# Kernel tuning notes

Measured on AMD Instinct MI355X. Metric: run time of the kernel, lower is better.

The kernel has to match this reference:

```python
import jax, jax.numpy as jnp
import numpy as np

N, E = 10000, 30000
D_IN, E_DIM, H1, H2, C = 64, 16, 128, 64, 10


def setup_inputs() -> dict:
    key = jax.random.key(0)
    ks = jax.random.split(key, 12)
    x = jax.random.normal(ks[0], (N, D_IN), dtype=jnp.float32)
    edge_attr = jax.random.normal(ks[1], (E, E_DIM), dtype=jnp.float32)
    edge_index = jax.random.randint(ks[2], (2, E), 0, N, dtype=jnp.int64)
    # linear1: D_IN -> H1
    W1 = jax.random.normal(ks[3], (D_IN, H1), dtype=jnp.float32) / np.sqrt(D_IN)
    b1 = jnp.zeros((H1,), dtype=jnp.float32)
    # edge MLP 1: E_DIM -> H1*H2
    We1 = jax.random.normal(ks[4], (E_DIM, H1 * H2), dtype=jnp.float32) / np.sqrt(E_DIM)
    be1 = jnp.zeros((H1 * H2,), dtype=jnp.float32)
    root1 = jax.random.uniform(ks[5], (H1, H2), dtype=jnp.float32,
                               minval=-1.0 / np.sqrt(H1), maxval=1.0 / np.sqrt(H1))
    bias1 = jnp.zeros((H2,), dtype=jnp.float32)
    # edge MLP 2: E_DIM -> H2*C
    We2 = jax.random.normal(ks[6], (E_DIM, H2 * C), dtype=jnp.float32) / np.sqrt(E_DIM)
    be2 = jnp.zeros((H2 * C,), dtype=jnp.float32)
    root2 = jax.random.uniform(ks[7], (H2, C), dtype=jnp.float32,
                               minval=-1.0 / np.sqrt(H2), maxval=1.0 / np.sqrt(H2))
    bias2 = jnp.zeros((C,), dtype=jnp.float32)
    return {"x": x, "edge_attr": edge_attr, "edge_index": edge_index,
            "W1": W1, "b1": b1, "We1": We1, "be1": be1, "root1": root1, "bias1": bias1,
            "We2": We2, "be2": be2, "root2": root2, "bias2": bias2}


def _nnconv(h, src, dst, edge_attr, We, be, root, bias, c_in, c_out):
    # per-edge weight matrix from edge MLP: [E, c_in, c_out]
    W_e = (edge_attr @ We + be).reshape(-1, c_in, c_out)
    msg = jnp.einsum('ei,eio->eo', h[src], W_e)          # gather + batched matmul
    agg = jax.ops.segment_sum(msg, dst, num_segments=N)   # scatter-add to target nodes
    return agg + h @ root + bias


def reference(x, edge_attr, edge_index, W1, b1, We1, be1, root1, bias1,
              We2, be2, root2, bias2):
    src, dst = edge_index[0], edge_index[1]  # PyG: x_j = x[src], aggregate at dst
    h = jax.nn.relu(x @ W1 + b1)                               # [N, H1]
    h = jax.nn.relu(_nnconv(h, src, dst, edge_attr, We1, be1, root1, bias1, H1, H2))
    z = _nnconv(h, src, dst, edge_attr, We2, be2, root2, bias2, H2, C)
    return jax.nn.log_softmax(z, axis=1)
```

## Files before the change

### kernel.cpp

```cpp
#include <hip/hip_runtime.h>

#define N_NODES 10000
#define N_EDGES 30000
#define DIN     64
#define EDIM    16
#define H1      128
#define H2      64
#define C_OUT   10

typedef __bf16 bfrag __attribute__((ext_vector_type(8)));
typedef float  f32x4 __attribute__((ext_vector_type(4)));
typedef ushort ushort8 __attribute__((ext_vector_type(8)));

__device__ __forceinline__ ushort f2bf(float f) {
    union { float f; unsigned u; } x; x.f = f;
    unsigned r = x.u + 0x7fffu + ((x.u >> 16) & 1u);
    return (ushort)(r >> 16);
}
__device__ __forceinline__ float bf2f(ushort s) {
    union { unsigned u; float f; } x; x.u = ((unsigned)s) << 16;
    return x.f;
}

#define KA_B1   1250
#define KA_B2   (KA_B1 + 576)
#define KA_B3   (KA_B2 + 48)
__global__ __launch_bounds__(256) void kA_prep(
        const float* __restrict__ x, const float* __restrict__ W1,
        const float* __restrict__ b1,
        const float* __restrict__ We1, const float* __restrict__ root1,
        const float* __restrict__ be1,
        const float* __restrict__ We2, const float* __restrict__ be2,
        const float* __restrict__ root2,
        ushort* __restrict__ h_bf, ushort* __restrict__ B1t,
        ushort* __restrict__ B2t) {
    int t = threadIdx.x;
    int bx = blockIdx.x;
    if (bx < KA_B1) {
        __shared__ float w_lds[DIN * H1];
        __shared__ float b_lds[H1];
        __shared__ float x_lds[8][DIN];
        for (int idx = t; idx < DIN * H1 / 4; idx += 256)
            ((float4*)w_lds)[idx] = ((const float4*)W1)[idx];
        if (t < H1) b_lds[t] = b1[t];
        int n0 = bx * 8;
        if (t < 128) {
            int row = t >> 4, c4 = t & 15;
            int n = n0 + row;
            float4 v = make_float4(0.f, 0.f, 0.f, 0.f);
            if (n < N_NODES) v = ((const float4*)(x + (size_t)n * DIN))[c4];
            ((float4*)(x_lds[row]))[c4] = v;
        }
        __syncthreads();
        int nl = t >> 5;
        int o  = (t & 31) * 4;
        int n  = n0 + nl;
        float4 acc = *(const float4*)&b_lds[o];
        #pragma unroll 8
        for (int i = 0; i < DIN; ++i) {
            float xv = x_lds[nl][i];
            float4 w = *(const float4*)&w_lds[i * H1 + o];
            acc.x = fmaf(xv, w.x, acc.x);
            acc.y = fmaf(xv, w.y, acc.y);
            acc.z = fmaf(xv, w.z, acc.z);
            acc.w = fmaf(xv, w.w, acc.w);
        }
        if (n < N_NODES) {
            ushort4 s;
            s.x = f2bf(fmaxf(acc.x, 0.f));
            s.y = f2bf(fmaxf(acc.y, 0.f));
            s.z = f2bf(fmaxf(acc.z, 0.f));
            s.w = f2bf(fmaxf(acc.w, 0.f));
            *(ushort4*)&h_bf[(size_t)n * H1 + o] = s;
        }
    } else if (bx < KA_B2) {
        int idx = (bx - KA_B1) * 256 + t;
        int c = idx >> 7, i = idx & 127;
        float v;
        if (c < 1024) {
            int o = c >> 4, k = c & 15;
            v = We1[(size_t)k * (H1 * H2) + i * 64 + o];
        } else if (c < 1088) v = root1[i * 64 + (c - 1024)];
        else                 v = be1[i * 64 + (c - 1088)];
        B1t[idx] = f2bf(v);
    } else {
        int idx = (bx - KA_B2) * 256 + t;
        int c = idx >> 6, j = idx & 63;
        float v = 0.f;
        if (c < 160) {
            int cc = c >> 4, k = c & 15;
            v = We2[(size_t)k * 640 + j * 10 + cc];
        }
        else if (c < 170) v = be2[j * 10 + (c - 160)];
        else if (c < 180) v = root2[j * 10 + (c - 170)];
        B2t[idx] = f2bf(v);
    }
}

__global__ __launch_bounds__(256) void k3_mfma(
        const ushort* __restrict__ h_bf, const ushort* __restrict__ Bt,
        const float* __restrict__ bias1,
        ushort* __restrict__ G1t, float* __restrict__ hrb1, float* __restrict__ hb1,
        float* __restrict__ agg1, float* __restrict__ agg2) {
    int t = threadIdx.x;
    int wave = t >> 6, lane = t & 63;
    int quad = lane >> 4, lrow = lane & 15;
    int yy = blockIdx.y;
    int mx = blockIdx.x;
    if (yy == 5) {
        for (int i = mx * 256 + t; i < 160000; i += 79 * 256)
            ((float4*)agg1)[i] = make_float4(0.f, 0.f, 0.f, 0.f);
        for (int i = mx * 256 + t; i < 25000; i += 79 * 256)
            ((float4*)agg2)[i] = make_float4(0.f, 0.f, 0.f, 0.f);
    }
    int nbase = mx * 128 + wave * 32;
    int ar0 = nbase + lrow;       if (ar0 > N_NODES - 1) ar0 = N_NODES - 1;
    int ar1 = nbase + 16 + lrow;  if (ar1 > N_NODES - 1) ar1 = N_NODES - 1;
    bfrag A0[4], A1[4];
    #pragma unroll
    for (int kc4 = 0; kc4 < 4; ++kc4) {
        A0[kc4] = *reinterpret_cast<const bfrag*>(
            h_bf + (size_t)ar0 * 128 + kc4 * 32 + quad * 8);
        A1[kc4] = *reinterpret_cast<const bfrag*>(
            h_bf + (size_t)ar1 * 128 + kc4 * 32 + quad * 8);
    }
    #pragma unroll
    for (int hy = 0; hy < 3; ++hy) {
        int y = yy * 3 + hy;
        const ushort* bbase = Bt + (size_t)y * 64 * 128;
        f32x4 acc0[4] = {}, acc1[4] = {};
        #pragma unroll
        for (int kc4 = 0; kc4 < 4; ++kc4) {
            #pragma unroll
            for (int ct = 0; ct < 4; ++ct) {
                bfrag b = *reinterpret_cast<const bfrag*>(
                    bbase + (size_t)(ct * 16 + lrow) * 128 + kc4 * 32 + quad * 8);
                acc0[ct] = __builtin_amdgcn_mfma_f32_16x16x32_bf16(A0[kc4], b, acc0[ct], 0, 0, 0);
                acc1[ct] = __builtin_amdgcn_mfma_f32_16x16x32_bf16(A1[kc4], b, acc1[ct], 0, 0, 0);
            }
        }
        #pragma unroll
        for (int half = 0; half < 2; ++half) {
            int rbase = nbase + half * 16 + quad * 4;
            #pragma unroll
            for (int ct = 0; ct < 4; ++ct) {
                int col = ct * 16 + lrow;
                f32x4 a = half ? acc1[ct] : acc0[ct];
                #pragma unroll
                for (int r = 0; r < 4; ++r) {
                    int n = rbase + r;
                    if (n >= N_NODES) continue;
                    float v = a[r];
                    if (y < 16) {
                        G1t[(size_t)n * 1024 + y * 64 + col] = f2bf(v);
                    } else if (y == 16) {
                        hrb1[(size_t)n * 64 + col] = v + bias1[col];
                    } else {
                        hb1[(size_t)n * 64 + col] = v;
                    }
                }
            }
        }
    }
}

__global__ __launch_bounds__(256) void k4_edge1(
        const float* __restrict__ ea, const int* __restrict__ src_idx,
        const int* __restrict__ dst_idx, const ushort* __restrict__ G1t,
        const float* __restrict__ hb1, float* __restrict__ agg1) {
    int t = threadIdx.x;
    int e0 = blockIdx.x * 8 + (t >> 6) * 2;
    int o = t & 63;
    int s0 = src_idx[e0],     d0 = dst_idx[e0];
    int s1 = src_idx[e0 + 1], d1 = dst_idx[e0 + 1];
    const ushort* g0p = G1t + (size_t)s0 * 1024 + o * 16;
    const ushort* g1p = G1t + (size_t)s1 * 1024 + o * 16;
    ushort8 ga0 = *reinterpret_cast<const ushort8*>(g0p);
    ushort8 ga1 = *reinterpret_cast<const ushort8*>(g0p + 8);
    ushort8 gb0 = *reinterpret_cast<const ushort8*>(g1p);
    ushort8 gb1 = *reinterpret_cast<const ushort8*>(g1p + 8);
    float m0 = hb1[(size_t)s0 * 64 + o];
    float m1 = hb1[(size_t)s1 * 64 + o];
    const float* a0 = ea + (size_t)e0 * 16;
    const float* a1 = a0 + 16;
    #pragma unroll
    for (int k = 0; k < 8; ++k) {
        m0 = fmaf(a0[k], bf2f(ga0[k]), m0);
        m1 = fmaf(a1[k], bf2f(gb0[k]), m1);
    }
    #pragma unroll
    for (int k = 0; k < 8; ++k) {
        m0 = fmaf(a0[k + 8], bf2f(ga1[k]), m0);
        m1 = fmaf(a1[k + 8], bf2f(gb1[k]), m1);
    }
    atomicAdd(&agg1[(size_t)d0 * 64 + o], m0);
    atomicAdd(&agg1[(size_t)d1 * 64 + o], m1);
}

__global__ __launch_bounds__(256) void k56_mfma(
        const float* __restrict__ agg1, const float* __restrict__ hrb1,
        const ushort* __restrict__ B2t, const float* __restrict__ bias2,
        float* __restrict__ G2t, float* __restrict__ hb2, float* __restrict__ hr2) {
    int t = threadIdx.x;
    int wave = t >> 6, lane = t & 63;
    int quad = lane >> 4, lrow = lane & 15;
    int n0 = blockIdx.x * 64 + wave * 16;
    int arow = n0 + lrow; if (arow > N_NODES - 1) arow = N_NODES - 1;
    bfrag A[2];
    #pragma unroll
    for (int kk = 0; kk < 2; ++kk) {
        size_t off = (size_t)arow * 64 + kk * 32 + quad * 8;
        f32x4 p0 = *(const f32x4*)(agg1 + off);
        f32x4 p1 = *(const f32x4*)(agg1 + off + 4);
        f32x4 q0 = *(const f32x4*)(hrb1 + off);
        f32x4 q1 = *(const f32x4*)(hrb1 + off + 4);
        bfrag a;
        #pragma unroll
        for (int j = 0; j < 4; ++j) {
            a[j]     = (__bf16)fmaxf(p0[j] + q0[j], 0.f);
            a[j + 4] = (__bf16)fmaxf(p1[j] + q1[j], 0.f);
        }
        A[kk] = a;
    }
    #pragma unroll
    for (int y = 0; y < 3; ++y) {
        f32x4 acc[4] = {};
        #pragma unroll
        for (int kk = 0; kk < 2; ++kk) {
            #pragma unroll
            for (int ct = 0; ct < 4; ++ct) {
                bfrag b = *reinterpret_cast<const bfrag*>(
                    B2t + (size_t)(y * 64 + ct * 16 + lrow) * 64 + kk * 32 + quad * 8);
                acc[ct] = __builtin_amdgcn_mfma_f32_16x16x32_bf16(A[kk], b, acc[ct], 0, 0, 0);
            }
        }
        #pragma unroll
        for (int ct = 0; ct < 4; ++ct) {
            int cg = y * 64 + ct * 16 + lrow;
            #pragma unroll
            for (int r = 0; r < 4; ++r) {
                int n = n0 + quad * 4 + r;
                if (n >= N_NODES) continue;
                float v = acc[ct][r];
                if (cg < 160)      G2t[(size_t)n * 160 + cg] = v;
                else if (cg < 170) hb2[(size_t)n * 10 + (cg - 160)] = v;
                else if (cg < 180) hr2[(size_t)n * 10 + (cg - 170)] = v + bias2[cg - 170];
            }
        }
    }
}

__global__ __launch_bounds__(256) void k7_edge2(
        const float* __restrict__ ea, const int* __restrict__ src_idx,
        const int* __restrict__ dst_idx, const float* __restrict__ G2t,
        const float* __restrict__ hb2, float* __restrict__ agg2) {
    int tid = blockIdx.x * 256 + threadIdx.x;
    if (tid >= N_EDGES * 10) return;
    int e = tid / 10, c = tid - e * 10;
    int s = src_idx[e], d = dst_idx[e];
    float m = hb2[(size_t)s * 10 + c];
    const float* g = G2t + (size_t)s * 160 + c * 16;
    const float* a = ea + (size_t)e * 16;
    f32x4 g0 = *(const f32x4*)g,       g1 = *(const f32x4*)(g + 4);
    f32x4 g2 = *(const f32x4*)(g + 8), g3 = *(const f32x4*)(g + 12);
    f32x4 a0 = *(const f32x4*)a,       a1 = *(const f32x4*)(a + 4);
    f32x4 a2 = *(const f32x4*)(a + 8), a3 = *(const f32x4*)(a + 12);
    #pragma unroll
    for (int k = 0; k < 4; ++k) {
        m = fmaf(a0[k], g0[k], m);
        m = fmaf(a1[k], g1[k], m);
        m = fmaf(a2[k], g2[k], m);
        m = fmaf(a3[k], g3[k], m);
    }
    atomicAdd(&agg2[(size_t)d * 10 + c], m);
}

__global__ void k8_logsoftmax(const float* __restrict__ agg2, const float* __restrict__ hr2,
                              float* __restrict__ out) {
    int n = blockIdx.x * blockDim.x + threadIdx.x;
    if (n >= N_NODES) return;
    float z[10]; float m = -1e30f;
    #pragma unroll
    for (int c = 0; c < 10; ++c) {
        z[c] = agg2[(size_t)n * 10 + c] + hr2[(size_t)n * 10 + c];
        m = fmaxf(m, z[c]);
    }
    float s = 0.f;
    #pragma unroll
    for (int c = 0; c < 10; ++c) s += expf(z[c] - m);
    float ls = logf(s);
    #pragma unroll
    for (int c = 0; c < 10; ++c) out[(size_t)n * 10 + c] = z[c] - m - ls;
}

extern "C" void kernel_launch(void* const* d_in, const int* in_sizes, int n_in,
                              void* d_out, int out_size, void* d_ws, size_t ws_size,
                              hipStream_t stream) {
    const float* x     = (const float*)d_in[0];
    const float* ea    = (const float*)d_in[1];
    const int*   eidx  = (const int*)d_in[2];
    const float* W1    = (const float*)d_in[3];
    const float* b1    = (const float*)d_in[4];
    const float* We1   = (const float*)d_in[5];
    const float* be1   = (const float*)d_in[6];
    const float* root1 = (const float*)d_in[7];
    const float* bias1 = (const float*)d_in[8];
    const float* We2   = (const float*)d_in[9];
    const float* be2   = (const float*)d_in[10];
    const float* root2 = (const float*)d_in[11];
    const float* bias2 = (const float*)d_in[12];
    float* out = (float*)d_out;

    float* ws = (float*)d_ws;
    ushort* h_bf = (ushort*)ws;
    ushort* B1t  = (ushort*)(ws + 640000);
    ushort* B2t  = (ushort*)(ws + 713728);
    ushort* G1t  = (ushort*)(ws + 719872);
    float* hrb1 = ws + 719872 + 5120000;
    float* hb1  = hrb1 + 640000;
    float* agg1 = hb1  + 640000;
    float* agg2 = agg1 + 640000;
    float* G2t  = agg2 + 100000;
    float* hb2  = G2t  + 1600000;
    float* hr2  = hb2  + 100000;

    kA_prep<<<KA_B3, 256, 0, stream>>>(x, W1, b1, We1, root1, be1, We2, be2, root2,
                                       h_bf, B1t, B2t);
    k3_mfma<<<dim3(79, 6), 256, 0, stream>>>(h_bf, B1t, bias1, G1t, hrb1, hb1,
                                             agg1, agg2);
    k4_edge1<<<3750, 256, 0, stream>>>(ea, eidx, eidx + N_EDGES, G1t, hb1, agg1);
    k56_mfma<<<157, 256, 0, stream>>>(agg1, hrb1, B2t, bias2, G2t, hb2, hr2);
    k7_edge2<<<1172, 256, 0, stream>>>(ea, eidx, eidx + N_EDGES, G2t, hb2, agg2);
    k8_logsoftmax<<<40, 256, 0, stream>>>(agg2, hr2, out);
}
```

Baseline: 138.2 us.

## Seed aggregation buffers with root terms and process four edges per wave

```diff
diff --git a/kernel.cpp b/kernel.cpp
--- a/kernel.cpp
+++ b/kernel.cpp
@@ -100,19 +100,13 @@
 __global__ __launch_bounds__(256) void k3_mfma(
         const ushort* __restrict__ h_bf, const ushort* __restrict__ Bt,
         const float* __restrict__ bias1,
-        ushort* __restrict__ G1t, float* __restrict__ hrb1, float* __restrict__ hb1,
-        float* __restrict__ agg1, float* __restrict__ agg2) {
+        ushort* __restrict__ G1t, float* __restrict__ agg1,
+        float* __restrict__ hb1) {
     int t = threadIdx.x;
     int wave = t >> 6, lane = t & 63;
     int quad = lane >> 4, lrow = lane & 15;
     int yy = blockIdx.y;
     int mx = blockIdx.x;
-    if (yy == 5) {
-        for (int i = mx * 256 + t; i < 160000; i += 79 * 256)
-            ((float4*)agg1)[i] = make_float4(0.f, 0.f, 0.f, 0.f);
-        for (int i = mx * 256 + t; i < 25000; i += 79 * 256)
-            ((float4*)agg2)[i] = make_float4(0.f, 0.f, 0.f, 0.f);
-    }
     int nbase = mx * 128 + wave * 32;
     int ar0 = nbase + lrow;       if (ar0 > N_NODES - 1) ar0 = N_NODES - 1;
     int ar1 = nbase + 16 + lrow;  if (ar1 > N_NODES - 1) ar1 = N_NODES - 1;
@@ -154,7 +148,7 @@
                     if (y < 16) {
                         G1t[(size_t)n * 1024 + y * 64 + col] = f2bf(v);
                     } else if (y == 16) {
-                        hrb1[(size_t)n * 64 + col] = v + bias1[col];
+                        agg1[(size_t)n * 64 + col] = v + bias1[col];
                     } else {
                         hb1[(size_t)n * 64 + col] = v;
                     }
@@ -169,38 +163,41 @@
         const int* __restrict__ dst_idx, const ushort* __restrict__ G1t,
         const float* __restrict__ hb1, float* __restrict__ agg1) {
     int t = threadIdx.x;
-    int e0 = blockIdx.x * 8 + (t >> 6) * 2;
+    int e0 = blockIdx.x * 16 + (t >> 6) * 4;
     int o = t & 63;
-    int s0 = src_idx[e0],     d0 = dst_idx[e0];
-    int s1 = src_idx[e0 + 1], d1 = dst_idx[e0 + 1];
-    const ushort* g0p = G1t + (size_t)s0 * 1024 + o * 16;
-    const ushort* g1p = G1t + (size_t)s1 * 1024 + o * 16;
-    ushort8 ga0 = *reinterpret_cast<const ushort8*>(g0p);
-    ushort8 ga1 = *reinterpret_cast<const ushort8*>(g0p + 8);
-    ushort8 gb0 = *reinterpret_cast<const ushort8*>(g1p);
-    ushort8 gb1 = *reinterpret_cast<const ushort8*>(g1p + 8);
-    float m0 = hb1[(size_t)s0 * 64 + o];
-    float m1 = hb1[(size_t)s1 * 64 + o];
-    const float* a0 = ea + (size_t)e0 * 16;
-    const float* a1 = a0 + 16;
-    #pragma unroll
-    for (int k = 0; k < 8; ++k) {
-        m0 = fmaf(a0[k], bf2f(ga0[k]), m0);
-        m1 = fmaf(a1[k], bf2f(gb0[k]), m1);
-    }
-    #pragma unroll
-    for (int k = 0; k < 8; ++k) {
-        m0 = fmaf(a0[k + 8], bf2f(ga1[k]), m0);
-        m1 = fmaf(a1[k + 8], bf2f(gb1[k]), m1);
-    }
-    atomicAdd(&agg1[(size_t)d0 * 64 + o], m0);
-    atomicAdd(&agg1[(size_t)d1 * 64 + o], m1);
+    int s[4], d[4];
+    #pragma unroll
+    for (int j = 0; j < 4; ++j) { s[j] = src_idx[e0 + j]; d[j] = dst_idx[e0 + j]; }
+    ushort8 g[4][2];
+    #pragma unroll
+    for (int j = 0; j < 4; ++j) {
+        const ushort* gp = G1t + (size_t)s[j] * 1024 + o * 16;
+        g[j][0] = *reinterpret_cast<const ushort8*>(gp);
+        g[j][1] = *reinterpret_cast<const ushort8*>(gp + 8);
+    }
+    float m[4];
+    #pragma unroll
+    for (int j = 0; j < 4; ++j) m[j] = hb1[(size_t)s[j] * 64 + o];
+    const float* a = ea + (size_t)e0 * 16;
+    #pragma unroll
+    for (int j = 0; j < 4; ++j) {
+        #pragma unroll
+        for (int k = 0; k < 8; ++k)
+            m[j] = fmaf(a[j * 16 + k], bf2f(g[j][0][k]), m[j]);
+        #pragma unroll
+        for (int k = 0; k < 8; ++k)
+            m[j] = fmaf(a[j * 16 + 8 + k], bf2f(g[j][1][k]), m[j]);
+    }
+    #pragma unroll
+    for (int j = 0; j < 4; ++j)
+        atomicAdd(&agg1[(size_t)d[j] * 64 + o], m[j]);
 }
 
 __global__ __launch_bounds__(256) void k56_mfma(
-        const float* __restrict__ agg1, const float* __restrict__ hrb1,
-        const ushort* __restrict__ B2t, const float* __restrict__ bias2,
-        float* __restrict__ G2t, float* __restrict__ hb2, float* __restrict__ hr2) {
+        const float* __restrict__ agg1, const ushort* __restrict__ B2t,
+        const float* __restrict__ bias2,
+        float* __restrict__ G2t, float* __restrict__ hb2,
+        float* __restrict__ agg2) {
     int t = threadIdx.x;
     int wave = t >> 6, lane = t & 63;
     int quad = lane >> 4, lrow = lane & 15;
@@ -212,13 +209,11 @@
         size_t off = (size_t)arow * 64 + kk * 32 + quad * 8;
         f32x4 p0 = *(const f32x4*)(agg1 + off);
         f32x4 p1 = *(const f32x4*)(agg1 + off + 4);
-        f32x4 q0 = *(const f32x4*)(hrb1 + off);
-        f32x4 q1 = *(const f32x4*)(hrb1 + off + 4);
         bfrag a;
         #pragma unroll
         for (int j = 0; j < 4; ++j) {
-            a[j]     = (__bf16)fmaxf(p0[j] + q0[j], 0.f);
-            a[j + 4] = (__bf16)fmaxf(p1[j] + q1[j], 0.f);
+            a[j]     = (__bf16)fmaxf(p0[j], 0.f);
+            a[j + 4] = (__bf16)fmaxf(p1[j], 0.f);
         }
         A[kk] = a;
     }
@@ -244,7 +239,7 @@
                 float v = acc[ct][r];
                 if (cg < 160)      G2t[(size_t)n * 160 + cg] = v;
                 else if (cg < 170) hb2[(size_t)n * 10 + (cg - 160)] = v;
-                else if (cg < 180) hr2[(size_t)n * 10 + (cg - 170)] = v + bias2[cg - 170];
+                else if (cg < 180) agg2[(size_t)n * 10 + (cg - 170)] = v + bias2[cg - 170];
             }
         }
     }
@@ -275,14 +270,14 @@
     atomicAdd(&agg2[(size_t)d * 10 + c], m);
 }
 
-__global__ void k8_logsoftmax(const float* __restrict__ agg2, const float* __restrict__ hr2,
+__global__ void k8_logsoftmax(const float* __restrict__ agg2,
                               float* __restrict__ out) {
     int n = blockIdx.x * blockDim.x + threadIdx.x;
     if (n >= N_NODES) return;
     float z[10]; float m = -1e30f;
     #pragma unroll
     for (int c = 0; c < 10; ++c) {
-        z[c] = agg2[(size_t)n * 10 + c] + hr2[(size_t)n * 10 + c];
+        z[c] = agg2[(size_t)n * 10 + c];
         m = fmaxf(m, z[c]);
     }
     float s = 0.f;
@@ -316,20 +311,17 @@
     ushort* B1t  = (ushort*)(ws + 640000);
     ushort* B2t  = (ushort*)(ws + 713728);
     ushort* G1t  = (ushort*)(ws + 719872);
-    float* hrb1 = ws + 719872 + 5120000;
-    float* hb1  = hrb1 + 640000;
+    float* hb1  = ws + 719872 + 5120000;
     float* agg1 = hb1  + 640000;
     float* agg2 = agg1 + 640000;
     float* G2t  = agg2 + 100000;
     float* hb2  = G2t  + 1600000;
-    float* hr2  = hb2  + 100000;
 
     kA_prep<<<KA_B3, 256, 0, stream>>>(x, W1, b1, We1, root1, be1, We2, be2, root2,
                                        h_bf, B1t, B2t);
-    k3_mfma<<<dim3(79, 6), 256, 0, stream>>>(h_bf, B1t, bias1, G1t, hrb1, hb1,
-                                             agg1, agg2);
-    k4_edge1<<<3750, 256, 0, stream>>>(ea, eidx, eidx + N_EDGES, G1t, hb1, agg1);
-    k56_mfma<<<157, 256, 0, stream>>>(agg1, hrb1, B2t, bias2, G2t, hb2, hr2);
+    k3_mfma<<<dim3(79, 6), 256, 0, stream>>>(h_bf, B1t, bias1, G1t, agg1, hb1);
+    k4_edge1<<<1875, 256, 0, stream>>>(ea, eidx, eidx + N_EDGES, G1t, hb1, agg1);
+    k56_mfma<<<157, 256, 0, stream>>>(agg1, B2t, bias2, G2t, hb2, agg2);
     k7_edge2<<<1172, 256, 0, stream>>>(ea, eidx, eidx + N_EDGES, G2t, hb2, agg2);
-    k8_logsoftmax<<<40, 256, 0, stream>>>(agg2, hr2, out);
-}
+    k8_logsoftmax<<<40, 256, 0, stream>>>(agg2, out);
+}
```

New measurement: 142.2 us. +2.9%, slower.

## Seed aggregation buffers with root terms, store G2 in bf16, batch W1 prep

Applied to the files above, without the earlier changes.

```diff
diff --git a/kernel.cpp b/kernel.cpp
--- a/kernel.cpp
+++ b/kernel.cpp
@@ -22,7 +22,7 @@
     return x.f;
 }
 
-#define KA_B1   1250
+#define KA_B1   313
 #define KA_B2   (KA_B1 + 576)
 #define KA_B3   (KA_B2 + 48)
 __global__ __launch_bounds__(256) void kA_prep(
@@ -43,35 +43,39 @@
         for (int idx = t; idx < DIN * H1 / 4; idx += 256)
             ((float4*)w_lds)[idx] = ((const float4*)W1)[idx];
         if (t < H1) b_lds[t] = b1[t];
-        int n0 = bx * 8;
-        if (t < 128) {
-            int row = t >> 4, c4 = t & 15;
-            int n = n0 + row;
-            float4 v = make_float4(0.f, 0.f, 0.f, 0.f);
-            if (n < N_NODES) v = ((const float4*)(x + (size_t)n * DIN))[c4];
-            ((float4*)(x_lds[row]))[c4] = v;
-        }
-        __syncthreads();
-        int nl = t >> 5;
-        int o  = (t & 31) * 4;
-        int n  = n0 + nl;
-        float4 acc = *(const float4*)&b_lds[o];
-        #pragma unroll 8
-        for (int i = 0; i < DIN; ++i) {
-            float xv = x_lds[nl][i];
-            float4 w = *(const float4*)&w_lds[i * H1 + o];
-            acc.x = fmaf(xv, w.x, acc.x);
-            acc.y = fmaf(xv, w.y, acc.y);
-            acc.z = fmaf(xv, w.z, acc.z);
-            acc.w = fmaf(xv, w.w, acc.w);
-        }
-        if (n < N_NODES) {
-            ushort4 s;
-            s.x = f2bf(fmaxf(acc.x, 0.f));
-            s.y = f2bf(fmaxf(acc.y, 0.f));
-            s.z = f2bf(fmaxf(acc.z, 0.f));
-            s.w = f2bf(fmaxf(acc.w, 0.f));
-            *(ushort4*)&h_bf[(size_t)n * H1 + o] = s;
+        #pragma unroll
+        for (int sub = 0; sub < 4; ++sub) {
+            int n0 = bx * 32 + sub * 8;
+            if (t < 128) {
+                int row = t >> 4, c4 = t & 15;
+                int n = n0 + row;
+                float4 v = make_float4(0.f, 0.f, 0.f, 0.f);
+                if (n < N_NODES) v = ((const float4*)(x + (size_t)n * DIN))[c4];
+                ((float4*)(x_lds[row]))[c4] = v;
+            }
+            __syncthreads();
+            int nl = t >> 5;
+            int o  = (t & 31) * 4;
+            int n  = n0 + nl;
+            float4 acc = *(const float4*)&b_lds[o];
+            #pragma unroll 8
+            for (int i = 0; i < DIN; ++i) {
+                float xv = x_lds[nl][i];
+                float4 w = *(const float4*)&w_lds[i * H1 + o];
+                acc.x = fmaf(xv, w.x, acc.x);
+                acc.y = fmaf(xv, w.y, acc.y);
+                acc.z = fmaf(xv, w.z, acc.z);
+                acc.w = fmaf(xv, w.w, acc.w);
+            }
+            if (n < N_NODES) {
+                ushort4 s;
+                s.x = f2bf(fmaxf(acc.x, 0.f));
+                s.y = f2bf(fmaxf(acc.y, 0.f));
+                s.z = f2bf(fmaxf(acc.z, 0.f));
+                s.w = f2bf(fmaxf(acc.w, 0.f));
+                *(ushort4*)&h_bf[(size_t)n * H1 + o] = s;
+            }
+            __syncthreads();
         }
     } else if (bx < KA_B2) {
         int idx = (bx - KA_B1) * 256 + t;
@@ -100,19 +104,13 @@
 __global__ __launch_bounds__(256) void k3_mfma(
         const ushort* __restrict__ h_bf, const ushort* __restrict__ Bt,
         const float* __restrict__ bias1,
-        ushort* __restrict__ G1t, float* __restrict__ hrb1, float* __restrict__ hb1,
-        float* __restrict__ agg1, float* __restrict__ agg2) {
+        ushort* __restrict__ G1t, float* __restrict__ agg1,
+        float* __restrict__ hb1) {
     int t = threadIdx.x;
     int wave = t >> 6, lane = t & 63;
     int quad = lane >> 4, lrow = lane & 15;
     int yy = blockIdx.y;
     int mx = blockIdx.x;
-    if (yy == 5) {
-        for (int i = mx * 256 + t; i < 160000; i += 79 * 256)
-            ((float4*)agg1)[i] = make_float4(0.f, 0.f, 0.f, 0.f);
-        for (int i = mx * 256 + t; i < 25000; i += 79 * 256)
-            ((float4*)agg2)[i] = make_float4(0.f, 0.f, 0.f, 0.f);
-    }
     int nbase = mx * 128 + wave * 32;
     int ar0 = nbase + lrow;       if (ar0 > N_NODES - 1) ar0 = N_NODES - 1;
     int ar1 = nbase + 16 + lrow;  if (ar1 > N_NODES - 1) ar1 = N_NODES - 1;
@@ -154,7 +152,7 @@
                     if (y < 16) {
                         G1t[(size_t)n * 1024 + y * 64 + col] = f2bf(v);
                     } else if (y == 16) {
-                        hrb1[(size_t)n * 64 + col] = v + bias1[col];
+                        agg1[(size_t)n * 64 + col] = v + bias1[col];
                     } else {
                         hb1[(size_t)n * 64 + col] = v;
                     }
@@ -198,9 +196,10 @@
 }
 
 __global__ __launch_bounds__(256) void k56_mfma(
-        const float* __restrict__ agg1, const float* __restrict__ hrb1,
-        const ushort* __restrict__ B2t, const float* __restrict__ bias2,
-        float* __restrict__ G2t, float* __restrict__ hb2, float* __restrict__ hr2) {
+        const float* __restrict__ agg1, const ushort* __restrict__ B2t,
+        const float* __restrict__ bias2,
+        ushort* __restrict__ G2t, float* __restrict__ hb2,
+        float* __restrict__ agg2) {
     int t = threadIdx.x;
     int wave = t >> 6, lane = t & 63;
     int quad = lane >> 4, lrow = lane & 15;
@@ -212,13 +211,11 @@
         size_t off = (size_t)arow * 64 + kk * 32 + quad * 8;
         f32x4 p0 = *(const f32x4*)(agg1 + off);
         f32x4 p1 = *(const f32x4*)(agg1 + off + 4);
-        f32x4 q0 = *(const f32x4*)(hrb1 + off);
-        f32x4 q1 = *(const f32x4*)(hrb1 + off + 4);
         bfrag a;
         #pragma unroll
         for (int j = 0; j < 4; ++j) {
-            a[j]     = (__bf16)fmaxf(p0[j] + q0[j], 0.f);
-            a[j + 4] = (__bf16)fmaxf(p1[j] + q1[j], 0.f);
+            a[j]     = (__bf16)fmaxf(p0[j], 0.f);
+            a[j + 4] = (__bf16)fmaxf(p1[j], 0.f);
         }
         A[kk] = a;
     }
@@ -242,9 +239,9 @@
                 int n = n0 + quad * 4 + r;
                 if (n >= N_NODES) continue;
                 float v = acc[ct][r];
-                if (cg < 160)      G2t[(size_t)n * 160 + cg] = v;
+                if (cg < 160)      G2t[(size_t)n * 160 + cg] = f2bf(v);
                 else if (cg < 170) hb2[(size_t)n * 10 + (cg - 160)] = v;
-                else if (cg < 180) hr2[(size_t)n * 10 + (cg - 170)] = v + bias2[cg - 170];
+                else if (cg < 180) agg2[(size_t)n * 10 + (cg - 170)] = v + bias2[cg - 170];
             }
         }
     }
@@ -252,37 +249,37 @@
 
 __global__ __launch_bounds__(256) void k7_edge2(
         const float* __restrict__ ea, const int* __restrict__ src_idx,
-        const int* __restrict__ dst_idx, const float* __restrict__ G2t,
+        const int* __restrict__ dst_idx, const ushort* __restrict__ G2t,
         const float* __restrict__ hb2, float* __restrict__ agg2) {
     int tid = blockIdx.x * 256 + threadIdx.x;
     if (tid >= N_EDGES * 10) return;
     int e = tid / 10, c = tid - e * 10;
     int s = src_idx[e], d = dst_idx[e];
     float m = hb2[(size_t)s * 10 + c];
-    const float* g = G2t + (size_t)s * 160 + c * 16;
+    const ushort* g = G2t + (size_t)s * 160 + c * 16;
+    ushort8 g0 = *reinterpret_cast<const ushort8*>(g);
+    ushort8 g1 = *reinterpret_cast<const ushort8*>(g + 8);
     const float* a = ea + (size_t)e * 16;
-    f32x4 g0 = *(const f32x4*)g,       g1 = *(const f32x4*)(g + 4);
-    f32x4 g2 = *(const f32x4*)(g + 8), g3 = *(const f32x4*)(g + 12);
     f32x4 a0 = *(const f32x4*)a,       a1 = *(const f32x4*)(a + 4);
     f32x4 a2 = *(const f32x4*)(a + 8), a3 = *(const f32x4*)(a + 12);
     #pragma unroll
     for (int k = 0; k < 4; ++k) {
-        m = fmaf(a0[k], g0[k], m);
-        m = fmaf(a1[k], g1[k], m);
-        m = fmaf(a2[k], g2[k], m);
-        m = fmaf(a3[k], g3[k], m);
+        m = fmaf(a0[k], bf2f(g0[k]), m);
+        m = fmaf(a1[k], bf2f(g0[k + 4]), m);
+        m = fmaf(a2[k], bf2f(g1[k]), m);
+        m = fmaf(a3[k], bf2f(g1[k + 4]), m);
     }
     atomicAdd(&agg2[(size_t)d * 10 + c], m);
 }
 
-__global__ void k8_logsoftmax(const float* __restrict__ agg2, const float* __restrict__ hr2,
+__global__ void k8_logsoftmax(const float* __restrict__ agg2,
                               float* __restrict__ out) {
     int n = blockIdx.x * blockDim.x + threadIdx.x;
     if (n >= N_NODES) return;
     float z[10]; float m = -1e30f;
     #pragma unroll
     for (int c = 0; c < 10; ++c) {
-        z[c] = agg2[(size_t)n * 10 + c] + hr2[(size_t)n * 10 + c];
+        z[c] = agg2[(size_t)n * 10 + c];
         m = fmaxf(m, z[c]);
     }
     float s = 0.f;
@@ -310,26 +307,25 @@
     const float* root2 = (const float*)d_in[11];
     const float* bias2 = (const float*)d_in[12];
     float* out = (float*)d_out;
+    const int* src_idx = eidx;
+    const int* dst_idx = eidx + N_EDGES;
 
     float* ws = (float*)d_ws;
     ushort* h_bf = (ushort*)ws;
     ushort* B1t  = (ushort*)(ws + 640000);
     ushort* B2t  = (ushort*)(ws + 713728);
     ushort* G1t  = (ushort*)(ws + 719872);
-    float* hrb1 = ws + 719872 + 5120000;
-    float* hb1  = hrb1 + 640000;
+    float* hb1  = ws + 719872 + 5120000;
     float* agg1 = hb1  + 640000;
     float* agg2 = agg1 + 640000;
-    float* G2t  = agg2 + 100000;
-    float* hb2  = G2t  + 1600000;
-    float* hr2  = hb2  + 100000;
-
-    kA_prep<<<KA_B3, 256, 0, stream>>>(x, W1, b1, We1, root1, be1, We2, be2, root2,
-                                       h_bf, B1t, B2t);
-    k3_mfma<<<dim3(79, 6), 256, 0, stream>>>(h_bf, B1t, bias1, G1t, hrb1, hb1,
-                                             agg1, agg2);
-    k4_edge1<<<3750, 256, 0, stream>>>(ea, eidx, eidx + N_EDGES, G1t, hb1, agg1);
-    k56_mfma<<<157, 256, 0, stream>>>(agg1, hrb1, B2t, bias2, G2t, hb2, hr2);
-    k7_edge2<<<1172, 256, 0, stream>>>(ea, eidx, eidx + N_EDGES, G2t, hb2, agg2);
-    k8_logsoftmax<<<40, 256, 0, stream>>>(agg2, hr2, out);
-}
+    ushort* G2t = (ushort*)(agg2 + 100000);
+    float* hb2  = agg2 + 100000 + 800000;
+
+    kA_prep<<<KA_B3, 256, 0, stream>>>(x, W1, b1, We1, root1, be1,
+                                       We2, be2, root2, h_bf, B1t, B2t);
+    k3_mfma<<<dim3(79, 6), 256, 0, stream>>>(h_bf, B1t, bias1, G1t, agg1, hb1);
+    k4_edge1<<<3750, 256, 0, stream>>>(ea, src_idx, dst_idx, G1t, hb1, agg1);
+    k56_mfma<<<157, 256, 0, stream>>>(agg1, B2t, bias2, G2t, hb2, agg2);
+    k7_edge2<<<1172, 256, 0, stream>>>(ea, src_idx, dst_idx, G2t, hb2, agg2);
+    k8_logsoftmax<<<40, 256, 0, stream>>>(agg2, out);
+}
```

After: 139.0 us. About the same (+0.6%).
